# Optimization experiments

Measured on AMD Instinct MI355X. Metric: run time of the kernel, lower is better.

The kernel has to match this reference:

```python
import jax, jax.numpy as jnp
import numpy as np

D_MODEL = 512
D_INNER = 1024   # expand * d_model
D_STATE = 16
D_CONV = 4
DT_RANK = 32     # ceil(d_model / 16)
BATCH = 8
SEQ = 1024


def _mamba(x, in_w, conv_w, conv_b, xp_w, dt_w, dt_b, A_log, Dp, out_w):
    # x: [B, L, d_model]
    Bb, Ls, _ = x.shape
    u, z = jnp.split(x @ in_w.T, 2, axis=-1)          # each [B, L, d_inner]
    # causal depthwise conv1d, kernel D_CONV, left-padded then truncated to L
    up = jnp.pad(u, ((0, 0), (D_CONV - 1, 0), (0, 0)))
    uc = conv_b + sum(up[:, k:k + Ls, :] * conv_w[:, k] for k in range(D_CONV))
    u = jax.nn.silu(uc)
    dbl = u @ xp_w.T                                   # [B, L, dt_rank+2*d_state]
    dt, Bm, Cm = jnp.split(dbl, [DT_RANK, DT_RANK + D_STATE], axis=-1)
    delta = jax.nn.softplus(dt @ dt_w.T + dt_b)        # [B, L, d_inner]
    A = -jnp.exp(A_log)                                # [d_inner, d_state]

    def step(h, inp):
        d_t, B_t, C_t, u_t = inp                       # [B,di],[B,ds],[B,ds],[B,di]
        h = h * jnp.exp(d_t[..., None] * A) + (d_t * u_t)[..., None] * B_t[:, None, :]
        return h, jnp.einsum('bds,bs->bd', h, C_t)

    h0 = jnp.zeros((Bb, D_INNER, D_STATE), x.dtype)
    xs = tuple(jnp.swapaxes(a, 0, 1) for a in (delta, Bm, Cm, u))
    _, ys = jax.lax.scan(step, h0, xs)                 # ys: [L, B, d_inner]
    y = jnp.swapaxes(ys, 0, 1) + u * Dp
    return (y * jax.nn.silu(z)) @ out_w.T              # [B, L, d_model]


def _params(key):
    ks = jax.random.split(key, 5)
    s = 0.02
    return {
        'in_w': jax.random.normal(ks[0], (2 * D_INNER, D_MODEL)) * s,
        'conv_w': jax.random.normal(ks[1], (D_INNER, D_CONV)) * 0.3,
        'conv_b': jnp.zeros((D_INNER,)),
        'xp_w': jax.random.normal(ks[2], (DT_RANK + 2 * D_STATE, D_INNER)) * s,
        'dt_w': jax.random.normal(ks[3], (D_INNER, DT_RANK)) * (DT_RANK ** -0.5),
        'dt_b': jnp.full((D_INNER,), -4.0),
        'A_log': jnp.log(jnp.tile(jnp.arange(1, D_STATE + 1, dtype=jnp.float32), (D_INNER, 1))),
        'D': jnp.ones((D_INNER,)),
        'out_w': jax.random.normal(ks[4], (D_MODEL, D_INNER)) * s,
    }


def setup_inputs():
    key = jax.random.key(0)
    kx, kf, kb = jax.random.split(key, 3)
    inp = {'x': jax.random.normal(kx, (BATCH, SEQ, D_MODEL), dtype=jnp.float32)}
    for n, v in _params(kf).items():
        inp[n + '_f'] = v
    for n, v in _params(kb).items():
        inp[n + '_b'] = v
    return inp


def reference(x, in_w_f, conv_w_f, conv_b_f, xp_w_f, dt_w_f, dt_b_f, A_log_f, D_f, out_w_f,
              in_w_b, conv_w_b, conv_b_b, xp_w_b, dt_w_b, dt_b_b, A_log_b, D_b, out_w_b):
    fwd = _mamba(x, in_w_f, conv_w_f, conv_b_f, xp_w_f, dt_w_f, dt_b_f, A_log_f, D_f, out_w_f)
    bwd = _mamba(x[:, ::-1, :], in_w_b, conv_w_b, conv_b_b, xp_w_b, dt_w_b, dt_b_b,
                 A_log_b, D_b, out_w_b)[:, ::-1, :]
    return fwd + bwd
```

## Files before the change

### kernel.cpp

```cpp
#include <hip/hip_runtime.h>
#include <math.h>

#define BATCH 8
#define SEQ 1024
#define D_MODEL 512
#define D_INNER 1024
#define D_STATE 16
#define DT_RANK 32
#define NROWS (BATCH * SEQ)
#define CH 64
#define CL 16
#define USLAB 8388608l

typedef short short8 __attribute__((ext_vector_type(8)));
typedef float f32x4 __attribute__((ext_vector_type(4)));

__device__ __forceinline__ float sigmoidf_(float x) { return 1.f / (1.f + __expf(-x)); }

__device__ __forceinline__ float softplus_(float v) {
  return (v > 20.f) ? v : __logf(1.f + __expf(v));
}

__device__ __forceinline__ ushort f2b(float f) {
  uint u = __float_as_uint(f);
  return (ushort)((u + 0x7FFFu + ((u >> 16) & 1u)) >> 16);
}
__device__ __forceinline__ float b2f(ushort u) {
  return __uint_as_float(((uint)u) << 16);
}

__device__ __forceinline__ void gload16(const ushort* g, const ushort* l) {
  __builtin_amdgcn_global_load_lds(
      (const __attribute__((address_space(1))) void*)g,
      (__attribute__((address_space(3))) void*)l, 16, 0, 0);
}

__device__ __forceinline__ int revrow(int m) {
  return (m & ~1023) | (1023 - (m & 1023));
}

template<int BM, int BN, int RW, int CW, int EPI, int DUALK, int MDIAG>
__global__ __launch_bounds__(256) void gemm_bf16(
    const ushort* __restrict__ A, int lda, const ushort* __restrict__ A2,
    const ushort* __restrict__ B, int ldb, const ushort* __restrict__ B2,
    float* __restrict__ Cf, ushort* __restrict__ Cb, ushort* __restrict__ Cb2,
    int ldc, int K, const float* __restrict__ bias, const float* __restrict__ bias2,
    int b_stride, int revC, int accumC)
{
  constexpr int MI = BM / RW / 16;
  constexpr int NJ = BN / CW / 16;
  __shared__ ushort As[2][BM * 32];
  __shared__ ushort Bs[2][BN * 32];
  const int tid = threadIdx.x;
  const int w = tid >> 6, lane = tid & 63;

  const int nwg = gridDim.x * gridDim.y;
  int bid = blockIdx.y * gridDim.x + blockIdx.x;
  int wgid = (bid & 7) * (nwg >> 3) + (bid >> 3);
  const int bm = (wgid / gridDim.x) * BM;
  const int bn = (wgid % gridDim.x) * BN;

  if (MDIAG) {
    int mdir = (bm >= NROWS) ? 1 : 0;
    B += mdir * b_stride;
    if (mdir) bias = bias2;
  }

  const int rw0 = (w / CW) * (MI * 16);
  const int cw0 = (w % CW) * (NJ * 16);
  const int srow = w * 16 + (lane >> 2);
  const int scol = (((lane & 3) ^ ((lane >> 3) & 3)) << 3);
  const int rchunk = (((lane >> 4) ^ (((lane & 15) >> 1) & 3)) << 3);

  f32x4 acc[MI][NJ] = {};

  auto stage = [&](int buf, int k0) {
    const ushort* Ap = A;
    const ushort* Bp = B;
    int kc = k0;
    bool hi = false;
    if (DUALK && k0 >= (K >> 1)) { Ap = A2; Bp = B2; kc = k0 - (K >> 1); hi = true; }
#pragma unroll
    for (int it = 0; it < BM / 64; ++it) {
      int gm = bm + it * 64 + srow;
      int arow = (DUALK && hi) ? revrow(gm) : gm;
      gload16(Ap + (long)arow * lda + kc + scol, &As[buf][(it * 64 + w * 16) * 32]);
    }
#pragma unroll
    for (int it = 0; it < BN / 64; ++it) {
      int gn = bn + it * 64 + srow;
      gload16(Bp + (long)gn * ldb + kc + scol, &Bs[buf][(it * 64 + w * 16) * 32]);
    }
  };

  stage(0, 0);
  __syncthreads();

  for (int k0 = 0; k0 < K; k0 += 32) {
    int cur = (k0 >> 5) & 1;
    if (k0 + 32 < K) stage(cur ^ 1, k0 + 32);
    short8 a[MI], b[NJ];
#pragma unroll
    for (int i = 0; i < MI; ++i)
      a[i] = *(const short8*)&As[cur][(rw0 + i * 16 + (lane & 15)) * 32 + rchunk];
#pragma unroll
    for (int j = 0; j < NJ; ++j)
      b[j] = *(const short8*)&Bs[cur][(cw0 + j * 16 + (lane & 15)) * 32 + rchunk];
#pragma unroll
    for (int i = 0; i < MI; ++i)
#pragma unroll
      for (int j = 0; j < NJ; ++j)
        acc[i][j] = __builtin_amdgcn_mfma_f32_16x16x32_bf16(a[i], b[j], acc[i][j], 0, 0, 0);
    __syncthreads();
  }

#pragma unroll
  for (int i = 0; i < MI; ++i)
#pragma unroll
    for (int r = 0; r < 4; ++r) {
      int m = bm + rw0 + i * 16 + (lane >> 4) * 4 + r;
      int crow = revC ? revrow(m) : m;
#pragma unroll
      for (int j = 0; j < NJ; ++j) {
        int n = bn + cw0 + j * 16 + (lane & 15);
        float v = acc[i][j][r];
        if (EPI == 0) {
          float* p = Cf + (long)crow * ldc + n;
          if (accumC) *p += v; else *p = v;
        } else if (EPI == 1) {
          Cb[(long)crow * ldc + n] = f2b(softplus_(v + bias[n]));
        } else if (EPI == 2) {
          int dir = n >> 11;
          int nn = n & 2047;
          int sub = nn & 1023;
          int row = dir ? revrow(m) : m;
          if (nn < D_INNER)
            Cb[dir * USLAB + (long)row * 1024 + sub] = f2b(v);
          else
            Cb2[dir * USLAB + (long)row * 1024 + sub] = f2b(v * sigmoidf_(v));
        } else {
          Cb[(long)crow * ldc + n] = f2b(v);
        }
      }
    }
}

struct Seg { const float4* s; ushort4* d; int n4; int bstart; };
struct ConvArgs { Seg seg[9]; };

__global__ __launch_bounds__(256) void convert_all(ConvArgs a)
{
  int blk = blockIdx.x;
  int i = 0;
#pragma unroll
  for (int k = 1; k < 9; ++k) if (blk >= a.seg[k].bstart) i = k;
  int idx = (blk - a.seg[i].bstart) * 256 + threadIdx.x;
  if (idx >= a.seg[i].n4) return;
  float4 v = a.seg[i].s[idx];
  ushort4 o;
  o.x = f2b(v.x); o.y = f2b(v.y); o.z = f2b(v.z); o.w = f2b(v.w);
  a.seg[i].d[idx] = o;
}

__global__ __launch_bounds__(256) void conv_silu(
    const ushort* __restrict__ u_bf,
    const float* __restrict__ cw_f, const float* __restrict__ cw_b,
    const float* __restrict__ cb_f, const float* __restrict__ cb_b,
    ushort* __restrict__ uc_bf)
{
  long i = (long)blockIdx.x * 256 + threadIdx.x;
  int dir = (int)(i >> 21);
  int r = (int)(i >> 8) & 8191;
  int d0 = ((int)i & 255) << 2;
  int t = r & (SEQ - 1);
  const float* cw = dir ? cw_b : cw_f;
  const float* cb = dir ? cb_b : cb_f;
  const ushort* p = u_bf + dir * USLAB + (long)r * D_INNER + d0;
  ushort4 u0 = *(const ushort4*)p;
  ushort4 u1 = (t >= 1) ? *(const ushort4*)(p - 1024) : ushort4{0, 0, 0, 0};
  ushort4 u2 = (t >= 2) ? *(const ushort4*)(p - 2048) : ushort4{0, 0, 0, 0};
  ushort4 u3 = (t >= 3) ? *(const ushort4*)(p - 3072) : ushort4{0, 0, 0, 0};
  float4 bb = *(const float4*)(cb + d0);
  float ub0[4] = {b2f(u0.x), b2f(u0.y), b2f(u0.z), b2f(u0.w)};
  float ub1[4] = {b2f(u1.x), b2f(u1.y), b2f(u1.z), b2f(u1.w)};
  float ub2[4] = {b2f(u2.x), b2f(u2.y), b2f(u2.z), b2f(u2.w)};
  float ub3[4] = {b2f(u3.x), b2f(u3.y), b2f(u3.z), b2f(u3.w)};
  float bbv[4] = {bb.x, bb.y, bb.z, bb.w};
  ushort ov[4];
#pragma unroll
  for (int j = 0; j < 4; ++j) {
    float4 wj = *(const float4*)(cw + (d0 + j) * 4);
    float acc = bbv[j];
    acc = fmaf(wj.w, ub0[j], acc);
    acc = fmaf(wj.z, ub1[j], acc);
    acc = fmaf(wj.y, ub2[j], acc);
    acc = fmaf(wj.x, ub3[j], acc);
    ov[j] = f2b(acc * sigmoidf_(acc));
  }
  ushort4 o;
  o.x = ov[0]; o.y = ov[1]; o.z = ov[2]; o.w = ov[3];
  *(ushort4*)(uc_bf + dir * USLAB + (long)r * D_INNER + d0) = o;
}

#define EP_FAST(dt, Ep)                                        \
  {                                                            \
    float E1 = __expf(-(dt));                                  \
    float E2 = E1 * E1, E4 = E2 * E2, E8 = E4 * E4;            \
    Ep[0] = E1;  Ep[1] = E2;      Ep[2] = E2 * E1;             \
    Ep[3] = E4;  Ep[4] = E4 * E1; Ep[5] = E4 * E2;             \
    Ep[6] = E4 * Ep[2]; Ep[7] = E8;  Ep[8] = E8 * E1;          \
    Ep[9] = E8 * E2; Ep[10] = E8 * Ep[2]; Ep[11] = E8 * E4;    \
    Ep[12] = E8 * Ep[4]; Ep[13] = E8 * Ep[5];                  \
    Ep[14] = E8 * Ep[6]; Ep[15] = E8 * E8;                     \
  }

__device__ __forceinline__ bool a_is_arange(const float* Ar) {
  bool ok = true;
#pragma unroll
  for (int s = 0; s < D_STATE; ++s)
    ok = ok && (fabsf(Ar[s] + (float)(s + 1)) <= 1e-3f * (float)(s + 1));
  return ok;
}

__global__ __launch_bounds__(256) void scan_partA(
    const ushort* __restrict__ delta_bf,
    const ushort* __restrict__ ucv_bf,
    const ushort* __restrict__ dblb,
    const float* __restrict__ A_log_f, const float* __restrict__ A_log_b,
    ushort* __restrict__ hend,
    float* __restrict__ dtsum_buf)
{
  __shared__ float bc[CL][16];
  long idx = (long)blockIdx.x * 256 + threadIdx.x;
  int d = (int)idx & 1023;
  int c = ((int)idx >> 10) & (CH - 1);
  int b = ((int)idx >> 16) & 7;
  int dir = (int)(idx >> 19);
  const long r0 = (long)b * SEQ + c * CL;
  const ushort* dblp = dblb + (long)dir * NROWS * 64;
  {
    int tt = threadIdx.x >> 4, ss = threadIdx.x & 15;
    bc[tt][ss] = b2f(dblp[(r0 + tt) * 64 + 32 + ss]);
  }
  const float* Alog = dir ? A_log_b : A_log_f;
  const ushort* dp = delta_bf + dir * USLAB;
  const ushort* up = ucv_bf + dir * USLAB;
  float Ar[D_STATE];
#pragma unroll
  for (int s = 0; s < D_STATE; ++s) Ar[s] = -__expf(Alog[d * D_STATE + s]);
  const bool fast = a_is_arange(Ar);
  float h[D_STATE] = {0.f};
  float dtsum = 0.f;
  __syncthreads();

  if (fast) {
    for (int t = 0; t < CL; ++t) {
      long r = r0 + t;
      float dt = b2f(dp[r * 1024 + d]);
      float u  = b2f(up[r * 1024 + d]);
      float du = dt * u;
      dtsum += dt;
      float Ep[16];
      EP_FAST(dt, Ep);
#pragma unroll
      for (int s = 0; s < D_STATE; ++s)
        h[s] = fmaf(h[s], Ep[s], du * bc[t][s]);
    }
  } else {
    for (int t = 0; t < CL; ++t) {
      long r = r0 + t;
      float dt = b2f(dp[r * 1024 + d]);
      float u  = b2f(up[r * 1024 + d]);
      float du = dt * u;
      dtsum += dt;
#pragma unroll
      for (int s = 0; s < D_STATE; ++s)
        h[s] = fmaf(h[s], __expf(dt * Ar[s]), du * bc[t][s]);
    }
  }
  long base = ((long)((dir * 8 + b) * CH + c) * D_STATE) * 1024 + d;
#pragma unroll
  for (int s = 0; s < D_STATE; ++s) hend[base + s * 1024] = f2b(h[s]);
  dtsum_buf[(long)((dir * 8 + b) * CH + c) * 1024 + d] = dtsum;
}

__global__ __launch_bounds__(256) void scan_partB(
    ushort* __restrict__ hend,
    const float* __restrict__ dtsum_buf,
    const float* __restrict__ A_log_f, const float* __restrict__ A_log_b)
{
  long idx = (long)blockIdx.x * 256 + threadIdx.x;
  int d = (int)idx & 1023;
  int s = ((int)idx >> 10) & 15;
  int b = ((int)idx >> 14) & 7;
  int dir = (int)(idx >> 17);
  const float* Alog = dir ? A_log_b : A_log_f;
  float Ars = -__expf(Alog[d * D_STATE + s]);
  float H = 0.f;
  for (int c = 0; c < CH; ++c) {
    long off = ((long)((dir * 8 + b) * CH + c) * D_STATE + s) * 1024 + d;
    float he = b2f(hend[off]);
    float P = __expf(Ars * dtsum_buf[(long)((dir * 8 + b) * CH + c) * 1024 + d]);
    hend[off] = f2b(H);
    H = fmaf(P, H, he);
  }
}

__global__ __launch_bounds__(256) void scan_partC(
    const ushort* __restrict__ delta_bf,
    const ushort* __restrict__ ucv_bf,
    const ushort* __restrict__ dblb,
    const float* __restrict__ A_log_f, const float* __restrict__ A_log_b,
    const float* __restrict__ Dp_f, const float* __restrict__ Dp_b,
    const ushort* __restrict__ zsilu_bf,
    const ushort* __restrict__ hinit,
    ushort* __restrict__ ydz_bf)
{
  __shared__ float bc[CL][32];
  long idx = (long)blockIdx.x * 256 + threadIdx.x;
  int d = (int)idx & 1023;
  int c = ((int)idx >> 10) & (CH - 1);
  int b = ((int)idx >> 16) & 7;
  int dir = (int)(idx >> 19);
  const long r0 = (long)b * SEQ + c * CL;
  const ushort* dblp = dblb + (long)dir * NROWS * 64;
  {
    int tt = threadIdx.x >> 4, cc = (threadIdx.x & 15) * 2;
    ushort2 v = *(const ushort2*)&dblp[(r0 + tt) * 64 + 32 + cc];
    bc[tt][cc] = b2f(v.x); bc[tt][cc + 1] = b2f(v.y);
  }
  const float* Alog = dir ? A_log_b : A_log_f;
  const ushort* dp = delta_bf + dir * USLAB;
  const ushort* up = ucv_bf + dir * USLAB;
  const ushort* zp = zsilu_bf + dir * USLAB;
  ushort* yp = ydz_bf + dir * USLAB;
  float Ar[D_STATE];
#pragma unroll
  for (int s = 0; s < D_STATE; ++s) Ar[s] = -__expf(Alog[d * D_STATE + s]);
  const bool fast = a_is_arange(Ar);
  float h[D_STATE];
  long base = ((long)((dir * 8 + b) * CH + c) * D_STATE) * 1024 + d;
#pragma unroll
  for (int s = 0; s < D_STATE; ++s) h[s] = b2f(hinit[base + s * 1024]);
  float Dd = (dir ? Dp_b : Dp_f)[d];
  __syncthreads();

  if (fast) {
    for (int t = 0; t < CL; ++t) {
      long r = r0 + t;
      float dt = b2f(dp[r * 1024 + d]);
      float u  = b2f(up[r * 1024 + d]);
      float du = dt * u;
      float Ep[16];
      EP_FAST(dt, Ep);
      float y = 0.f;
#pragma unroll
      for (int s = 0; s < D_STATE; ++s) {
        h[s] = fmaf(h[s], Ep[s], du * bc[t][s]);
        y = fmaf(h[s], bc[t][16 + s], y);
      }
      float zs = b2f(zp[r * 1024 + d]);
      float yv = fmaf(u, Dd, y);
      yp[r * 1024 + d] = f2b(yv * zs);
    }
  } else {
    for (int t = 0; t < CL; ++t) {
      long r = r0 + t;
      float dt = b2f(dp[r * 1024 + d]);
      float u  = b2f(up[r * 1024 + d]);
      float du = dt * u;
      float y = 0.f;
#pragma unroll
      for (int s = 0; s < D_STATE; ++s) {
        h[s] = fmaf(h[s], __expf(dt * Ar[s]), du * bc[t][s]);
        y = fmaf(h[s], bc[t][16 + s], y);
      }
      float zs = b2f(zp[r * 1024 + d]);
      float yv = fmaf(u, Dd, y);
      yp[r * 1024 + d] = f2b(yv * zs);
    }
  }
}

extern "C" void kernel_launch(void* const* d_in, const int* in_sizes, int n_in,
                              void* d_out, int out_size, void* d_ws, size_t ws_size,
                              hipStream_t stream)
{
  const float* x = (const float*)d_in[0];
  float* out = (float*)d_out;
  char* ws = (char*)d_ws;
  ushort* zsilu  = (ushort*)(ws);
  ushort* ucv    = (ushort*)(ws + (32ul << 20));
  ushort* u_bf   = (ushort*)(ws + (64ul << 20));
  ushort* hend   = (ushort*)(ws + (96ul << 20));
  float*  dtsum  = (float*)(ws + (128ul << 20));
  ushort* dblb   = (ushort*)(ws + (132ul << 20));
  ushort* out_wb = (ushort*)(ws + (134ul << 20));
  ushort* xbf    = hend;
  ushort* in_wb  = hend + (8ul << 19);
  ushort* xp_wb  = hend + (12ul << 19);
  ushort* dt_wb  = xp_wb + 131072;
  ushort* delta  = u_bf;
  ushort* ydz    = ucv;

  ConvArgs ca;
  int bcur = 0, si = 0;
  auto addseg = [&](const float* s, ushort* d, int nelem) {
    ca.seg[si].s = (const float4*)s; ca.seg[si].d = (ushort4*)d;
    ca.seg[si].n4 = nelem / 4; ca.seg[si].bstart = bcur;
    bcur += (nelem / 4 + 255) / 256; ++si;
  };
  addseg(x, xbf, NROWS * D_MODEL);
  addseg((const float*)d_in[1], in_wb, 2048 * 512);
  addseg((const float*)d_in[10], in_wb + 2048 * 512, 2048 * 512);
  addseg((const float*)d_in[9], out_wb, 512 * 1024);
  addseg((const float*)d_in[18], out_wb + 512 * 1024, 512 * 1024);
  addseg((const float*)d_in[4], xp_wb, 64 * 1024);
  addseg((const float*)d_in[13], xp_wb + 65536, 64 * 1024);
  addseg((const float*)d_in[5], dt_wb, 1024 * 32);
  addseg((const float*)d_in[14], dt_wb + 32768, 1024 * 32);

  dim3 blk(256);
  convert_all<<<dim3(bcur), blk, 0, stream>>>(ca);

  gemm_bf16<128, 128, 2, 2, 2, 0, 0><<<dim3(32, 64), blk, 0, stream>>>(
      xbf, D_MODEL, nullptr, in_wb, D_MODEL, nullptr,
      nullptr, u_bf, zsilu, 0, D_MODEL, nullptr, nullptr, 0, 0, 0);
  conv_silu<<<dim3(2 * NROWS), blk, 0, stream>>>(
      u_bf, (const float*)d_in[2], (const float*)d_in[11],
      (const float*)d_in[3], (const float*)d_in[12], ucv);
  gemm_bf16<64, 64, 2, 2, 4, 0, 1><<<dim3(1, 256), blk, 0, stream>>>(
      ucv, D_INNER, nullptr, xp_wb, D_INNER, nullptr,
      nullptr, dblb, nullptr, 64, D_INNER, nullptr, nullptr, 65536, 0, 0);
  gemm_bf16<128, 128, 2, 2, 1, 0, 1><<<dim3(8, 128), blk, 0, stream>>>(
      dblb, 64, nullptr, dt_wb, DT_RANK, nullptr,
      nullptr, delta, nullptr, D_INNER, DT_RANK,
      (const float*)d_in[6], (const float*)d_in[15], 32768, 0, 0);
  const float* Alf = (const float*)d_in[7];
  const float* Alb = (const float*)d_in[16];
  scan_partA<<<dim3(2 * BATCH * CH * 1024 / 256), blk, 0, stream>>>(
      delta, ucv, dblb, Alf, Alb, hend, dtsum);
  scan_partB<<<dim3(2 * BATCH * 16 * 1024 / 256), blk, 0, stream>>>(
      hend, dtsum, Alf, Alb);
  scan_partC<<<dim3(2 * BATCH * CH * 1024 / 256), blk, 0, stream>>>(
      delta, ucv, dblb, Alf, Alb,
      (const float*)d_in[8], (const float*)d_in[17], zsilu, hend, ydz);
  gemm_bf16<128, 128, 2, 2, 0, 1, 0><<<dim3(4, 64), blk, 0, stream>>>(
      ydz, D_INNER, ydz + USLAB, out_wb, D_INNER, out_wb + 512 * 1024,
      out, nullptr, nullptr, D_MODEL, 2 * D_INNER, nullptr, nullptr, 0, 0, 0);
}
```

Before: 257.7 us.

## Add dedicated 256x256-tile triple-buffered in-projection GEMM kernel

Replaces the generic 128x128 bf16 GEMM used for the input projection with a specialized kernel using 256x256 tiles, 512 threads (8 waves), and a three-stage LDS pipeline with direct global-to-LDS loads. Loads for future k-tiles are interleaved between MFMA phases, with priority raised around the MFMA blocks. The aim is more operand reuse per tile and better overlap of global loads with compute. In exchange it uses much more LDS and registers (8x4 accumulators per wave), which can lower occupancy, and the grid drops to 512 workgroups.

```diff
diff --git a/kernel.cpp b/kernel.cpp
--- a/kernel.cpp
+++ b/kernel.cpp
@@ -37,6 +37,110 @@
 
 __device__ __forceinline__ int revrow(int m) {
   return (m & ~1023) | (1023 - (m & 1023));
+}
+
+__global__ __launch_bounds__(512, 2) void inproj256(
+    const ushort* __restrict__ A, int lda,
+    const ushort* __restrict__ B, int ldb,
+    ushort* __restrict__ Cu, ushort* __restrict__ Cz,
+    int K)
+{
+  __shared__ ushort As[3][256 * 32];
+  __shared__ ushort Bs[3][256 * 32];
+  const int tid = threadIdx.x;
+  const int w = tid >> 6, lane = tid & 63;
+
+  const int nwg = gridDim.x * gridDim.y;
+  int bid = blockIdx.y * gridDim.x + blockIdx.x;
+  int wgid = (bid & 7) * (nwg >> 3) + (bid >> 3);
+  const int bm = (wgid / gridDim.x) * 256;
+  const int bn = (wgid % gridDim.x) * 256;
+
+  const int wr = w >> 2, wc = w & 3;
+  const int rw0 = wr * 128, cw0 = wc * 64;
+  const int srow = w * 16 + (lane >> 2);
+  const int scol = (((lane & 3) ^ ((lane >> 3) & 3)) << 3);
+  const int rchunk = (((lane >> 4) ^ (((lane & 15) >> 1) & 3)) << 3);
+
+  f32x4 acc[8][4] = {};
+
+  auto stageA = [&](int buf, int k0, int half) {
+    int gm = bm + half * 128 + srow;
+    gload16(A + (long)gm * lda + k0 + scol, &As[buf][(half * 128 + w * 16) * 32]);
+  };
+  auto stageB = [&](int buf, int k0, int half) {
+    int gn = bn + half * 128 + srow;
+    gload16(B + (long)gn * ldb + k0 + scol, &Bs[buf][(half * 128 + w * 16) * 32]);
+  };
+
+  const int NT = K >> 5;
+  stageA(0, 0, 0); stageA(0, 0, 1); stageB(0, 0, 0); stageB(0, 0, 1);
+  stageA(1, 32, 0); stageA(1, 32, 1); stageB(1, 32, 0); stageB(1, 32, 1);
+  asm volatile("s_waitcnt vmcnt(4)" ::: "memory");
+  __builtin_amdgcn_s_barrier();
+
+  int buf = 0;
+  for (int t = 0; t < NT; ++t) {
+    const int kf = (t + 2) << 5;
+    const int sbuf = (buf >= 1) ? buf - 1 : buf + 2;
+    short8 a0[4], b0[4];
+#pragma unroll
+    for (int i = 0; i < 4; ++i)
+      a0[i] = *(const short8*)&As[buf][(rw0 + i * 16 + (lane & 15)) * 32 + rchunk];
+#pragma unroll
+    for (int j = 0; j < 4; ++j)
+      b0[j] = *(const short8*)&Bs[buf][(cw0 + j * 16 + (lane & 15)) * 32 + rchunk];
+    if (t + 2 < NT) { stageA(sbuf, kf, 0); stageA(sbuf, kf, 1); }
+    __builtin_amdgcn_s_barrier();
+    __builtin_amdgcn_s_setprio(1);
+#pragma unroll
+    for (int i = 0; i < 4; ++i)
+#pragma unroll
+      for (int j = 0; j < 4; ++j)
+        acc[i][j] = __builtin_amdgcn_mfma_f32_16x16x32_bf16(a0[i], b0[j], acc[i][j], 0, 0, 0);
+    __builtin_amdgcn_s_setprio(0);
+    __builtin_amdgcn_s_barrier();
+    short8 a1[4];
+#pragma unroll
+    for (int i = 0; i < 4; ++i)
+      a1[i] = *(const short8*)&As[buf][(rw0 + 64 + i * 16 + (lane & 15)) * 32 + rchunk];
+    if (t + 2 < NT) {
+      stageB(sbuf, kf, 0); stageB(sbuf, kf, 1);
+      asm volatile("s_waitcnt vmcnt(4)" ::: "memory");
+    } else if (t + 1 < NT) {
+      asm volatile("s_waitcnt vmcnt(0)" ::: "memory");
+    }
+    __builtin_amdgcn_s_barrier();
+    __builtin_amdgcn_s_setprio(1);
+#pragma unroll
+    for (int i = 0; i < 4; ++i)
+#pragma unroll
+      for (int j = 0; j < 4; ++j)
+        acc[4 + i][j] = __builtin_amdgcn_mfma_f32_16x16x32_bf16(a1[i], b0[j], acc[4 + i][j], 0, 0, 0);
+    __builtin_amdgcn_s_setprio(0);
+    __builtin_amdgcn_s_barrier();
+    buf = (buf == 2) ? 0 : buf + 1;
+  }
+
+#pragma unroll
+  for (int i = 0; i < 8; ++i)
+#pragma unroll
+    for (int r = 0; r < 4; ++r) {
+      int m = bm + rw0 + i * 16 + (lane >> 4) * 4 + r;
+#pragma unroll
+      for (int j = 0; j < 4; ++j) {
+        int n = bn + cw0 + j * 16 + (lane & 15);
+        float v = acc[i][j][r];
+        int dir = n >> 11;
+        int nn = n & 2047;
+        int sub = nn & 1023;
+        int row = dir ? revrow(m) : m;
+        if (nn < D_INNER)
+          Cu[dir * USLAB + (long)row * 1024 + sub] = f2b(v);
+        else
+          Cz[dir * USLAB + (long)row * 1024 + sub] = f2b(v * sigmoidf_(v));
+      }
+    }
 }
 
 template<int BM, int BN, int RW, int CW, int EPI, int DUALK, int MDIAG>
@@ -423,9 +527,8 @@
   dim3 blk(256);
   convert_all<<<dim3(bcur), blk, 0, stream>>>(ca);
 
-  gemm_bf16<128, 128, 2, 2, 2, 0, 0><<<dim3(32, 64), blk, 0, stream>>>(
-      xbf, D_MODEL, nullptr, in_wb, D_MODEL, nullptr,
-      nullptr, u_bf, zsilu, 0, D_MODEL, nullptr, nullptr, 0, 0, 0);
+  inproj256<<<dim3(4096 / 256, NROWS / 256), dim3(512), 0, stream>>>(
+      xbf, D_MODEL, in_wb, D_MODEL, u_bf, zsilu, D_MODEL);
   conv_silu<<<dim3(2 * NROWS), blk, 0, stream>>>(
       u_bf, (const float*)d_in[2], (const float*)d_in[11],
       (const float*)d_in[3], (const float*)d_in[12], ucv);
```

After: 259.4 us. Within noise of the previous version (+0.7%).
